# Performance work log

Hardware: AMD Instinct MI355X
Metric: run time of the kernel (lower is better)

The kernel has to match this reference:

```python
import jax, jax.numpy as jnp
import numpy as np
import math

EXP_BASE = 2.0  # exponential base weighting higher-order cliques


def _coef(m, n_L):
    """Multinomial coefficients fac(m-1)/prod_c fac(count_c) over all n_L^m label
    tuples, in row-major (first index outermost) order, matching the flatten order
    of the original torch.ger chain and basis_mat construction. Returned reshaped
    to (n_L,)*m so it can be contracted directly with the outer products."""
    idx = np.stack(np.unravel_index(np.arange(n_L ** m), (n_L,) * m), axis=1)  # [n_L^m, m]
    fact = np.array([math.factorial(i) for i in range(m + 1)], dtype=np.float64)
    counts = np.stack([(idx == c).sum(1) for c in range(n_L)], axis=1)  # [n_L^m, n_L]
    c = math.factorial(m - 1) / np.prod(fact[counts], axis=1)
    return jnp.asarray(c.reshape((n_L,) * m).astype(np.float32))


def setup_inputs() -> dict:
    key = jax.random.key(0)
    k1, k2, k3, k4 = jax.random.split(key, 4)
    n_V, n_L, n_fixed = 100_000, 4, 10_000
    S2, S3 = 2_000_000, 1_000_000
    fixed_indices = jnp.arange(n_fixed, dtype=jnp.int32)
    # fixed nodes carry one-hot labels, as in the original x_known buffer
    fixed_labels = jax.random.randint(k1, (n_fixed,), 0, n_L)
    fixed_params = jnp.eye(n_L, dtype=jnp.float32)[fixed_labels]
    trainable_params = jax.random.normal(k2, (n_V - n_fixed, n_L), dtype=jnp.float32)
    simplices_2 = jax.random.randint(k3, (S2, 2), 0, n_V, dtype=jnp.int32)
    simplices_3 = jax.random.randint(k4, (S3, 3), 0, n_V, dtype=jnp.int32)
    return {
        "trainable_params": trainable_params,
        "fixed_params": fixed_params,
        "fixed_indices": fixed_indices,
        "simplices_2": simplices_2,
        "simplices_3": simplices_3,
    }


def reference(trainable_params, fixed_params, fixed_indices, simplices_2, simplices_3):
    n_fixed, n_L = fixed_params.shape
    n_V = n_fixed + trainable_params.shape[0]
    trainable_indices = jnp.arange(n_fixed, n_V)

    # 1) scatter fixed + trainable rows into the dense node matrix
    full = jnp.zeros((n_V, n_L), dtype=trainable_params.dtype)
    full = full.at[fixed_indices].set(fixed_params)
    full = full.at[trainable_indices].set(trainable_params)

    # 2) row softmax -> valid per-node class distributions
    P = jax.nn.softmax(full, axis=1)

    # 3) per-simplex generalized outer products contracted against the
    #    multinomial coefficient tensors (k=0 term has coef 0 and is skipped).
    coef2 = _coef(2, n_L)  # [L, L]
    coef3 = _coef(3, n_L)  # [L, L, L]
    g2 = P[simplices_2]    # [S2, 2, L] gather
    g3 = P[simplices_3]    # [S3, 3, L] gather
    obj2 = jnp.einsum('sa,sb,ab->', g2[:, 0], g2[:, 1], coef2)
    obj3 = jnp.einsum('sa,sb,sc,abc->', g3[:, 0], g3[:, 1], g3[:, 2], coef3)

    return EXP_BASE * obj2 + (EXP_BASE ** 2) * obj3
```

## Files before the change

kernel.cpp:

```cpp
#include <hip/hip_runtime.h>


#define NL 4

__device__ __forceinline__ float dot4(float4 a, float4 b) {
    return a.x * b.x + a.y * b.y + a.z * b.z + a.w * b.w;
}

__global__ void softmax_rows(const float* __restrict__ trainable,
                             const float* __restrict__ fixedp,
                             const int* __restrict__ fixed_idx,
                             float* __restrict__ P,
                             int n_fixed, int n_total) {
    int i = blockIdx.x * blockDim.x + threadIdx.x;
    if (i >= n_total) return;
    float4 v;
    int dst;
    if (i < n_fixed) {
        v = ((const float4*)fixedp)[i];
        dst = fixed_idx[i];
    } else {
        v = ((const float4*)trainable)[i - n_fixed];
        dst = i;
    }
    float m = fmaxf(fmaxf(v.x, v.y), fmaxf(v.z, v.w));
    float ex = __expf(v.x - m), ey = __expf(v.y - m);
    float ez = __expf(v.z - m), ew = __expf(v.w - m);
    float inv = 1.0f / (ex + ey + ez + ew);
    ((float4*)P)[dst] = make_float4(ex * inv, ey * inv, ez * inv, ew * inv);
}

__global__ void gather_reduce(const int* __restrict__ s2, int S2, int nb2,
                              const int* __restrict__ s3, int S3,
                              const float* __restrict__ P,
                              float* __restrict__ part2,
                              float* __restrict__ part3) {
    const float4* __restrict__ Pv = (const float4*)P;
    __shared__ float lds[8];
    int wid = threadIdx.x >> 6;

    if ((int)blockIdx.x < nb2) {
        int tid = blockIdx.x * blockDim.x + threadIdx.x;
        int base = tid * 4;
        float sum = 0.f;
        if (base + 4 <= S2) {
            const int4* s = (const int4*)s2;
            int4 a = s[tid * 2], b = s[tid * 2 + 1];
            float4 p0 = Pv[a.x], q0 = Pv[a.y];
            float4 p1 = Pv[a.z], q1 = Pv[a.w];
            float4 p2 = Pv[b.x], q2 = Pv[b.y];
            float4 p3 = Pv[b.z], q3 = Pv[b.w];
            sum = dot4(p0, q0) + dot4(p1, q1) + dot4(p2, q2) + dot4(p3, q3);
        } else {
            for (int e = base; e < S2; ++e)
                sum += dot4(Pv[s2[2 * e]], Pv[s2[2 * e + 1]]);
        }
        #pragma unroll
        for (int off = 32; off > 0; off >>= 1) sum += __shfl_down(sum, off, 64);
        if ((threadIdx.x & 63) == 0) lds[wid] = sum;
        __syncthreads();
        if (threadIdx.x == 0)
            part2[blockIdx.x] = lds[0] + lds[1] + lds[2] + lds[3];
    } else {
        int bb = blockIdx.x - nb2;
        int tid = bb * blockDim.x + threadIdx.x;
        int base = tid * 4;
        float s_uvw = 0.f, s_t = 0.f;
        if (base + 4 <= S3) {
            const int4* s = (const int4*)s3;
            int4 a = s[tid * 3], b = s[tid * 3 + 1], c = s[tid * 3 + 2];
            int i0[4] = {a.x, a.w, b.z, c.y};
            int i1[4] = {a.y, b.x, b.w, c.z};
            int i2[4] = {a.z, b.y, c.x, c.w};
            float4 pp[4], qq[4], rr[4];
            #pragma unroll
            for (int k = 0; k < 4; ++k) {
                pp[k] = Pv[i0[k]]; qq[k] = Pv[i1[k]]; rr[k] = Pv[i2[k]];
            }
            #pragma unroll
            for (int k = 0; k < 4; ++k) {
                float4 p = pp[k], q = qq[k], r = rr[k];
                s_uvw += dot4(p, q) + dot4(p, r) + dot4(q, r);
                s_t += p.x * q.x * r.x + p.y * q.y * r.y
                     + p.z * q.z * r.z + p.w * q.w * r.w;
            }
        } else {
            for (int e = base; e < S3; ++e) {
                float4 p = Pv[s3[3 * e]], q = Pv[s3[3 * e + 1]], r = Pv[s3[3 * e + 2]];
                s_uvw += dot4(p, q) + dot4(p, r) + dot4(q, r);
                s_t += p.x * q.x * r.x + p.y * q.y * r.y
                     + p.z * q.z * r.z + p.w * q.w * r.w;
            }
        }
        #pragma unroll
        for (int off = 32; off > 0; off >>= 1) {
            s_uvw += __shfl_down(s_uvw, off, 64);
            s_t   += __shfl_down(s_t,   off, 64);
        }
        if ((threadIdx.x & 63) == 0) { lds[wid] = s_uvw; lds[4 + wid] = s_t; }
        __syncthreads();
        if (threadIdx.x == 0) {
            part3[2 * bb]     = lds[0] + lds[1] + lds[2] + lds[3];
            part3[2 * bb + 1] = lds[4] + lds[5] + lds[6] + lds[7];
        }
    }
}

__global__ void final_combine(const float* __restrict__ part2, int nb2,
                              const float* __restrict__ part3, int nb3,
                              float* __restrict__ out, float S2f, float S3f) {
    float dot2 = 0.f, uvw = 0.f, t = 0.f;
    for (int i = threadIdx.x; i < nb2; i += 256) dot2 += part2[i];
    for (int i = threadIdx.x; i < nb3; i += 256) {
        uvw += part3[2 * i];
        t   += part3[2 * i + 1];
    }
    #pragma unroll
    for (int off = 32; off > 0; off >>= 1) {
        dot2 += __shfl_down(dot2, off, 64);
        uvw  += __shfl_down(uvw,  off, 64);
        t    += __shfl_down(t,    off, 64);
    }
    __shared__ float lds[12];
    int wid = threadIdx.x >> 6;
    if ((threadIdx.x & 63) == 0) {
        lds[wid] = dot2; lds[4 + wid] = uvw; lds[8 + wid] = t;
    }
    __syncthreads();
    if (threadIdx.x == 0) {
        float D = lds[0] + lds[1] + lds[2] + lds[3];
        float U = lds[4] + lds[5] + lds[6] + lds[7];
        float T = lds[8] + lds[9] + lds[10] + lds[11];
        float obj2 = S2f - 0.5f * D;
        float obj3 = 2.f * S3f - U + (4.f / 3.f) * T;
        out[0] = 2.f * obj2 + 4.f * obj3;
    }
}

extern "C" void kernel_launch(void* const* d_in, const int* in_sizes, int n_in,
                              void* d_out, int out_size, void* d_ws, size_t ws_size,
                              hipStream_t stream) {
    const float* trainable = (const float*)d_in[0];
    const float* fixedp    = (const float*)d_in[1];
    const int*   fixed_idx = (const int*)d_in[2];
    const int*   s2        = (const int*)d_in[3];
    const int*   s3        = (const int*)d_in[4];

    int n_fixed = in_sizes[2];
    int n_L     = in_sizes[1] / n_fixed;
    int n_train = in_sizes[0] / n_L;
    int n_V     = n_fixed + n_train;
    int S2      = in_sizes[3] / 2;
    int S3      = in_sizes[4] / 3;
    (void)n_L; (void)ws_size; (void)n_in; (void)out_size;

    float* P     = (float*)d_ws;
    float* part2 = P + (size_t)n_V * NL;
    int threads2 = (S2 + 3) / 4;
    int nb2      = (threads2 + 255) / 256;
    float* part3 = part2 + nb2;
    int threads3 = (S3 + 3) / 4;
    int nb3      = (threads3 + 255) / 256;

    softmax_rows<<<(n_V + 255) / 256, 256, 0, stream>>>(
        trainable, fixedp, fixed_idx, P, n_fixed, n_V);

    gather_reduce<<<nb2 + nb3, 256, 0, stream>>>(s2, S2, nb2, s3, S3, P,
                                                 part2, part3);

    final_combine<<<1, 256, 0, stream>>>(part2, nb2, part3, nb3,
                                         (float*)d_out, (float)S2, (float)S3);
}
```

Before: 112.4 us.

## Use persistent grid-stride gather-reduce with two simplices per thread

The gather-reduce kernel now launches a fixed grid of 2048 blocks. Each block strides over virtual blocks covering both the 2-simplex and 3-simplex work and keeps one running sum per thread across all of them, so there is a single reduction and partial write per block. Each thread now handles two simplices per iteration instead of four, which adds memory-level parallelism through more threads per item while giving fewer loads in flight per thread. Odd tail simplices are handled by one thread, and the final combine reads a fixed number of partials.

```diff
diff --git a/kernel.cpp b/kernel.cpp
--- a/kernel.cpp
+++ b/kernel.cpp
@@ -2,8 +2,11 @@
 
 
 #define NL 4
+#define GRB 2048
 
-__device__ __forceinline__ float dot4(float4 a, float4 b) {
+typedef float v4f __attribute__((ext_vector_type(4)));
+
+__device__ __forceinline__ float dot4(v4f a, v4f b) {
     return a.x * b.x + a.y * b.y + a.z * b.z + a.w * b.w;
 }
 
@@ -31,78 +34,73 @@
 }
 
 __global__ void gather_reduce(const int* __restrict__ s2, int S2, int nb2,
-                              const int* __restrict__ s3, int S3,
+                              const int* __restrict__ s3, int S3, int nbTot,
                               const float* __restrict__ P,
                               float* __restrict__ part2,
                               float* __restrict__ part3) {
-    const float4* __restrict__ Pv = (const float4*)P;
-    __shared__ float lds[8];
+    const v4f* __restrict__ Pv = (const v4f*)P;
+    __shared__ float lds[12];
     int wid = threadIdx.x >> 6;
 
-    if ((int)blockIdx.x < nb2) {
-        int tid = blockIdx.x * blockDim.x + threadIdx.x;
-        int base = tid * 4;
-        float sum = 0.f;
-        if (base + 4 <= S2) {
-            const int4* s = (const int4*)s2;
-            int4 a = s[tid * 2], b = s[tid * 2 + 1];
-            float4 p0 = Pv[a.x], q0 = Pv[a.y];
-            float4 p1 = Pv[a.z], q1 = Pv[a.w];
-            float4 p2 = Pv[b.x], q2 = Pv[b.y];
-            float4 p3 = Pv[b.z], q3 = Pv[b.w];
-            sum = dot4(p0, q0) + dot4(p1, q1) + dot4(p2, q2) + dot4(p3, q3);
+    const int U2 = S2 >> 1;
+    const int V3 = S3 >> 1;
+
+    float sum2 = 0.f, s_uvw = 0.f, s_t = 0.f;
+
+    for (int vb = blockIdx.x; vb < nbTot; vb += gridDim.x) {
+        if (vb < nb2) {
+            int u = vb * 256 + (int)threadIdx.x;
+            if (u < U2) {
+                int4 a = ((const int4*)s2)[u];
+                v4f p0 = Pv[a.x], q0 = Pv[a.y];
+                v4f p1 = Pv[a.z], q1 = Pv[a.w];
+                sum2 += dot4(p0, q0) + dot4(p1, q1);
+            }
         } else {
-            for (int e = base; e < S2; ++e)
-                sum += dot4(Pv[s2[2 * e]], Pv[s2[2 * e + 1]]);
-        }
-        #pragma unroll
-        for (int off = 32; off > 0; off >>= 1) sum += __shfl_down(sum, off, 64);
-        if ((threadIdx.x & 63) == 0) lds[wid] = sum;
-        __syncthreads();
-        if (threadIdx.x == 0)
-            part2[blockIdx.x] = lds[0] + lds[1] + lds[2] + lds[3];
-    } else {
-        int bb = blockIdx.x - nb2;
-        int tid = bb * blockDim.x + threadIdx.x;
-        int base = tid * 4;
-        float s_uvw = 0.f, s_t = 0.f;
-        if (base + 4 <= S3) {
-            const int4* s = (const int4*)s3;
-            int4 a = s[tid * 3], b = s[tid * 3 + 1], c = s[tid * 3 + 2];
-            int i0[4] = {a.x, a.w, b.z, c.y};
-            int i1[4] = {a.y, b.x, b.w, c.z};
-            int i2[4] = {a.z, b.y, c.x, c.w};
-            float4 pp[4], qq[4], rr[4];
-            #pragma unroll
-            for (int k = 0; k < 4; ++k) {
-                pp[k] = Pv[i0[k]]; qq[k] = Pv[i1[k]]; rr[k] = Pv[i2[k]];
-            }
-            #pragma unroll
-            for (int k = 0; k < 4; ++k) {
-                float4 p = pp[k], q = qq[k], r = rr[k];
+            int v = (vb - nb2) * 256 + (int)threadIdx.x;
+            if (v < V3) {
+                const int2* s = (const int2*)s3;
+                int2 a = s[3 * v], b = s[3 * v + 1], c = s[3 * v + 2];
+                v4f p = Pv[a.x], q = Pv[a.y], r = Pv[b.x];
                 s_uvw += dot4(p, q) + dot4(p, r) + dot4(q, r);
                 s_t += p.x * q.x * r.x + p.y * q.y * r.y
                      + p.z * q.z * r.z + p.w * q.w * r.w;
-            }
-        } else {
-            for (int e = base; e < S3; ++e) {
-                float4 p = Pv[s3[3 * e]], q = Pv[s3[3 * e + 1]], r = Pv[s3[3 * e + 2]];
+                p = Pv[b.y]; q = Pv[c.x]; r = Pv[c.y];
                 s_uvw += dot4(p, q) + dot4(p, r) + dot4(q, r);
                 s_t += p.x * q.x * r.x + p.y * q.y * r.y
                      + p.z * q.z * r.z + p.w * q.w * r.w;
             }
         }
-        #pragma unroll
-        for (int off = 32; off > 0; off >>= 1) {
-            s_uvw += __shfl_down(s_uvw, off, 64);
-            s_t   += __shfl_down(s_t,   off, 64);
+    }
+
+    if (blockIdx.x == 0 && threadIdx.x == 0) {
+        if (S2 & 1) {
+            int e = S2 - 1;
+            sum2 += dot4(Pv[s2[2 * e]], Pv[s2[2 * e + 1]]);
         }
-        if ((threadIdx.x & 63) == 0) { lds[wid] = s_uvw; lds[4 + wid] = s_t; }
-        __syncthreads();
-        if (threadIdx.x == 0) {
-            part3[2 * bb]     = lds[0] + lds[1] + lds[2] + lds[3];
-            part3[2 * bb + 1] = lds[4] + lds[5] + lds[6] + lds[7];
+        if (S3 & 1) {
+            int e = S3 - 1;
+            v4f p = Pv[s3[3 * e]], q = Pv[s3[3 * e + 1]], r = Pv[s3[3 * e + 2]];
+            s_uvw += dot4(p, q) + dot4(p, r) + dot4(q, r);
+            s_t += p.x * q.x * r.x + p.y * q.y * r.y
+                 + p.z * q.z * r.z + p.w * q.w * r.w;
         }
+    }
+
+    #pragma unroll
+    for (int off = 32; off > 0; off >>= 1) {
+        sum2  += __shfl_down(sum2,  off, 64);
+        s_uvw += __shfl_down(s_uvw, off, 64);
+        s_t   += __shfl_down(s_t,   off, 64);
+    }
+    if ((threadIdx.x & 63) == 0) {
+        lds[wid] = sum2; lds[4 + wid] = s_uvw; lds[8 + wid] = s_t;
+    }
+    __syncthreads();
+    if (threadIdx.x == 0) {
+        part2[blockIdx.x]         = lds[0] + lds[1] + lds[2] + lds[3];
+        part3[2 * blockIdx.x]     = lds[4] + lds[5] + lds[6] + lds[7];
+        part3[2 * blockIdx.x + 1] = lds[8] + lds[9] + lds[10] + lds[11];
     }
 }
 
@@ -156,18 +154,20 @@
 
     float* P     = (float*)d_ws;
     float* part2 = P + (size_t)n_V * NL;
-    int threads2 = (S2 + 3) / 4;
-    int nb2      = (threads2 + 255) / 256;
-    float* part3 = part2 + nb2;
-    int threads3 = (S3 + 3) / 4;
-    int nb3      = (threads3 + 255) / 256;
+    float* part3 = part2 + GRB;
+
+    int U2    = S2 >> 1;
+    int V3    = S3 >> 1;
+    int nb2   = (U2 + 255) / 256;
+    int nb3   = (V3 + 255) / 256;
+    int nbTot = nb2 + nb3;
 
     softmax_rows<<<(n_V + 255) / 256, 256, 0, stream>>>(
         trainable, fixedp, fixed_idx, P, n_fixed, n_V);
 
-    gather_reduce<<<nb2 + nb3, 256, 0, stream>>>(s2, S2, nb2, s3, S3, P,
-                                                 part2, part3);
+    gather_reduce<<<GRB, 256, 0, stream>>>(s2, S2, nb2, s3, S3, nbTot, P,
+                                           part2, part3);
 
-    final_combine<<<1, 256, 0, stream>>>(part2, nb2, part3, nb3,
+    final_combine<<<1, 256, 0, stream>>>(part2, GRB, part3, GRB,
                                          (float*)d_out, (float)S2, (float)S3);
 }
```

Result: no change. 112.6 us (+0.2%).
